# Performance work log

Measured on AMD Instinct MI355X. Metric: run time of the kernel, lower is better.

## Reference

```python
import jax, jax.numpy as jnp
import numpy as np

B, T, C_IN = 2, 4096, 1024
INTER, OUT = 1024, 1024
ROPE_DIM = 64
GAMMA = 0.99609375  # 1 - 2**-8
GROUPS = 32
EPS = 1e-6


def setup_inputs() -> dict:
    key = jax.random.key(0)
    k = jax.random.split(key, 4)
    return {
        "X_Q": jax.random.normal(k[0], (B, T, C_IN), dtype=jnp.float32),
        "W_Q": jax.random.normal(k[1], (C_IN, INTER), dtype=jnp.float32) / C_IN,
        "W_K": jax.random.normal(k[2], (C_IN, INTER), dtype=jnp.float32) / C_IN,
        "W_V": jax.random.normal(k[3], (C_IN, OUT), dtype=jnp.float32) / C_IN,
        "gn_weight": jnp.ones((OUT,), dtype=jnp.float32),
        "gn_bias": jnp.zeros((OUT,), dtype=jnp.float32),
    }


def _rope(x):
    # lucidrains RotaryEmbedding: rotate first ROPE_DIM features, pairwise-adjacent
    t = x.shape[-2]
    inv_freq = 1.0 / (10000.0 ** (jnp.arange(0, ROPE_DIM, 2, dtype=jnp.float32) / ROPE_DIM))
    freqs = jnp.arange(t, dtype=jnp.float32)[:, None] * inv_freq[None, :]  # [T, ROPE_DIM/2]
    freqs = jnp.repeat(freqs, 2, axis=-1)                                   # [T, ROPE_DIM]
    cos, sin = jnp.cos(freqs), jnp.sin(freqs)
    xr, xp = x[..., :ROPE_DIM], x[..., ROPE_DIM:]
    x1, x2 = xr[..., 0::2], xr[..., 1::2]
    rot = jnp.stack([-x2, x1], axis=-1).reshape(xr.shape)  # rotate_half (adjacent pairs)
    return jnp.concatenate([xr * cos + rot * sin, xp], axis=-1)


def _group_norm(x, w, b):
    # torch GroupNorm applied on x.reshape(-1, C)
    sh = x.shape
    c = sh[-1]
    xr = x.reshape(-1, GROUPS, c // GROUPS)
    mu = xr.mean(-1, keepdims=True)
    var = xr.var(-1, keepdims=True)
    xn = ((xr - mu) * jax.lax.rsqrt(var + EPS)).reshape(-1, c)
    return (xn * w + b).reshape(sh)


def reference(X_Q, W_Q, W_K, W_V, gn_weight, gn_bias):
    Q = jax.nn.silu(_rope(X_Q @ W_Q))  # [B,T,INTER]
    K = jax.nn.silu(_rope(X_Q @ W_K))
    V = jax.nn.silu(X_Q @ W_V)         # [B,T,OUT]
    A = jnp.einsum('btd,bsd->bts', Q, K)  # [B,T,T]
    # decay mask: original multiplies by _get_D(gamma,T).T -> gamma^(m-n) for m>=n
    n = jnp.arange(T)[:, None]
    m = jnp.arange(T)[None, :]
    upper = m >= n
    Dt = jnp.where(upper, GAMMA ** jnp.where(upper, m - n, 0).astype(jnp.float32), 0.0)
    A = A * Dt
    out = jnp.einsum('bts,bsd->btd', A, V)  # [B,T,OUT]
    # dropout p=0 (eval) -> identity
    return _group_norm(out, gn_weight, gn_bias)
```

## Files before the change

kernel.cpp:

```cpp
#include <hip/hip_runtime.h>


typedef __attribute__((ext_vector_type(8))) short bf16x8;
typedef __attribute__((ext_vector_type(4))) short bf16x4;
typedef __attribute__((ext_vector_type(4))) float f32x4;

#define MFMA16(a, b, c) __builtin_amdgcn_mfma_f32_16x16x32_bf16(a, b, c, 0, 0, 0)

static __device__ __forceinline__ short f2bf(float f) {
  unsigned u = __builtin_bit_cast(unsigned, f);
  u = (u + 0x7fffu + ((u >> 16) & 1u)) >> 16;
  return (short)u;
}

static __device__ __forceinline__ float fast_silu(float v) {
  return v * __builtin_amdgcn_rcpf(1.f + __expf(-v));
}

static __device__ __forceinline__ void gl_lds16(const void* g, void* l) {
  __builtin_amdgcn_global_load_lds(
      (const __attribute__((address_space(1))) void*)g,
      (__attribute__((address_space(3))) void*)l, 16, 0, 0);
}

static __device__ __forceinline__ int swzc(int col, int row) {
  return (((col >> 3) ^ (row & 7)) << 3) | (col & 7);
}

#define T_LEN 4096
#define CIN 1024

#define LOG2G (-0.0056465633f)
#define L2IF (0.41524101f)

__global__ __launch_bounds__(256)
void prep_kernel(const float* __restrict__ X, short* __restrict__ Xb,
                 const float* __restrict__ Wq, const float* __restrict__ Wk,
                 const float* __restrict__ Wv, short* __restrict__ WT) {
  __shared__ short tile[64][72];
  const int bx = blockIdx.x;
  const int tid = threadIdx.x;
  if (bx < 4096) {
    const int gid = bx * 256 + tid;
    const int row = gid >> 7;
    const int c = gid & 127;
    const float* s = &X[(size_t)gid * 8];
    float4 f0 = *(const float4*)s;
    float4 f1 = *(const float4*)(s + 4);
    bf16x8 v = {f2bf(f0.x), f2bf(f0.y), f2bf(f0.z), f2bf(f0.w),
                f2bf(f1.x), f2bf(f1.y), f2bf(f1.z), f2bf(f1.w)};
    const int pc = (c & 0x78) | ((c ^ row) & 7);
    *(bf16x8*)&Xb[(size_t)row * 1024 + pc * 8] = v;
    return;
  }
  const int bx2 = bx - 4096;
  const int k0 = (bx2 & 15) * 64, n0 = ((bx2 >> 4) & 15) * 64, mat = bx2 >> 8;
  const float* __restrict__ W = (mat == 0) ? Wq : (mat == 1) ? Wk : Wv;
  const int r = tid >> 4, c = tid & 15;
#pragma unroll
  for (int i = 0; i < 4; ++i) {
    int row = r + 16 * i;
    float4 f = *(const float4*)&W[(size_t)(k0 + row) * CIN + n0 + c * 4];
    tile[c * 4 + 0][row] = f2bf(f.x);
    tile[c * 4 + 1][row] = f2bf(f.y);
    tile[c * 4 + 2][row] = f2bf(f.z);
    tile[c * 4 + 3][row] = f2bf(f.w);
  }
  __syncthreads();
  const int n = tid >> 2, seg = tid & 3;
  bf16x8 lo = *(const bf16x8*)&tile[n][seg * 16];
  bf16x8 hi = *(const bf16x8*)&tile[n][seg * 16 + 8];
  const int R = mat * 1024 + n0 + n;
  const int a0 = (k0 >> 3) + seg * 2;
  short* base = &WT[(size_t)R * CIN];
  *(bf16x8*)&base[(a0 ^ (n & 7)) * 8] = lo;
  *(bf16x8*)&base[((a0 + 1) ^ (n & 7)) * 8] = hi;
}

#define GEMM_DECLS()                                   \
  const int tid = threadIdx.x;                         \
  const int lane = tid & 63, wave = tid >> 6;          \
  const int wm = wave >> 1, wn = wave & 1;             \
  const int l15 = lane & 15, quad = lane >> 4;         \
  const int srow = tid >> 3;                           \
  const int scol = (tid & 7) * 8;                      \
  const int asw = (l15 & 7);

#define ACC_INIT4(acc)                                 \
  _Pragma("unroll") for (int i = 0; i < 4; ++i)        \
  _Pragma("unroll") for (int j = 0; j < 4; ++j) {      \
    f32x4 z = {0.f, 0.f, 0.f, 0.f};                    \
    acc[i][j] = z;                                     \
  }

#define STAGE_TILE(dst, src, ld, r0, k0, nrows)        \
  _Pragma("unroll") for (int i = 0; i < (nrows) / 32; ++i) \
    gl_lds16(&src[(size_t)((r0) + i * 32 + srow) * (ld) + (k0) + scol], \
             &dst[i * 32 + srow][scol]);

#define FRAG_MFMA44(As, Bs, acc)                                            \
  {                                                                         \
    bf16x8 af[4][2], bfr[4][2];                                             \
    _Pragma("unroll") for (int im = 0; im < 4; ++im)                        \
    _Pragma("unroll") for (int ks = 0; ks < 2; ++ks)                        \
      af[im][ks] = *(const bf16x8*)&As[wm * 64 + im * 16 + l15]             \
                       [((ks * 4 + quad) ^ asw) * 8];                       \
    _Pragma("unroll") for (int in = 0; in < 4; ++in)                        \
    _Pragma("unroll") for (int ks = 0; ks < 2; ++ks)                        \
      bfr[in][ks] = *(const bf16x8*)&Bs[wn * 64 + in * 16 + l15]            \
                        [((ks * 4 + quad) ^ asw) * 8];                      \
    _Pragma("unroll") for (int ks = 0; ks < 2; ++ks)                        \
    _Pragma("unroll") for (int im = 0; im < 4; ++im)                        \
    _Pragma("unroll") for (int in = 0; in < 4; ++in)                        \
      acc[im][in] = MFMA16(af[im][ks], bfr[in][ks], acc[im][in]);           \
  }

__global__ __launch_bounds__(256, 2)
void qkv_gemm(const short* __restrict__ Xb, const short* __restrict__ WT,
              short* __restrict__ Qb, short* __restrict__ Kb,
              short* __restrict__ Vt) {
  __shared__ __align__(16) short As[128][64];
  __shared__ __align__(16) short Bs[128][64];
  GEMM_DECLS();
  const int m0 = blockIdx.x * 128;
  const int c0 = blockIdx.y * 128;

  f32x4 acc[4][4];
  ACC_INIT4(acc);

  for (int k0 = 0; k0 < CIN; k0 += 64) {
    __syncthreads();
    STAGE_TILE(As, Xb, CIN, m0, k0, 128);
    STAGE_TILE(Bs, WT, CIN, c0, k0, 128);
    __syncthreads();
    FRAG_MFMA44(As, Bs, acc);
  }

  const int mat = (c0 >> 10);
  const bool ropeBlk = (mat < 2) && ((c0 & 1023) == 0);
#pragma unroll
  for (int im = 0; im < 4; ++im) {
#pragma unroll
    for (int in = 0; in < 4; ++in) {
      const int c = c0 + wn * 64 + in * 16 + l15;
      const int colm = c & 1023;
      const int mbase = m0 + wm * 64 + im * 16 + quad * 4;
      short vv[4];
      if (ropeBlk && colm < 64) {
        const float invf = exp2f(-L2IF * (float)(colm >> 1));
#pragma unroll
        for (int r = 0; r < 4; ++r) {
          float v = acc[im][in][r];
          int t = (mbase + r) & (T_LEN - 1);
          float partner = __shfl_xor(v, 1, 64);
          float ang = (float)t * invf;
          float s_ = __sinf(ang), c_ = __cosf(ang);
          v = (colm & 1) ? (v * c_ + partner * s_) : (v * c_ - partner * s_);
          vv[r] = f2bf(fast_silu(v));
        }
      } else {
#pragma unroll
        for (int r = 0; r < 4; ++r) vv[r] = f2bf(fast_silu(acc[im][in][r]));
      }
      if (mat == 0) {
#pragma unroll
        for (int r = 0; r < 4; ++r)
          Qb[(size_t)(mbase + r) * 1024 + swzc(colm, mbase + r)] = vv[r];
      } else if (mat == 1) {
#pragma unroll
        for (int r = 0; r < 4; ++r)
          Kb[(size_t)(mbase + r) * 1024 + swzc(colm, mbase + r)] = vv[r];
      } else {
        bf16x4 v4 = {vv[0], vv[1], vv[2], vv[3]};
        *(bf16x4*)&Vt[(size_t)colm * 8192 +
                      (((mbase >> 3) ^ (colm & 7)) << 3) + (mbase & 7)] = v4;
      }
    }
  }
}

__global__ __launch_bounds__(256, 2)
void score_kernel(const short* __restrict__ Qb, const short* __restrict__ Kb,
                  short* __restrict__ Ab) {
  int idx = blockIdx.x;
  int ti = 0;
  while (idx >= 32 - ti) { idx -= 32 - ti; ++ti; }
  const int si = ti + idx;
  const int b = blockIdx.y;
  const int s0 = si * 128, t0 = ti * 128;

  __shared__ __align__(16) short Qs[128][64];
  __shared__ __align__(16) short Ks[128][64];
  GEMM_DECLS();

  f32x4 acc[4][4];
  ACC_INIT4(acc);

  for (int k0 = 0; k0 < 1024; k0 += 64) {
    __syncthreads();
    STAGE_TILE(Qs, Qb, 1024, b * T_LEN + t0, k0, 128);
    STAGE_TILE(Ks, Kb, 1024, b * T_LEN + s0, k0, 128);
    __syncthreads();
    FRAG_MFMA44(Qs, Ks, acc);
  }

#pragma unroll
  for (int im = 0; im < 4; ++im) {
#pragma unroll
    for (int in = 0; in < 4; ++in) {
      int s = s0 + wn * 64 + in * 16 + l15;
#pragma unroll
      for (int r = 0; r < 4; ++r) {
        int t = t0 + wm * 64 + im * 16 + quad * 4 + r;
        int d = s - t;
        float v = acc[im][in][r];
        v = (d < 0) ? 0.f : v * exp2f((float)d * LOG2G);
        Ab[((size_t)(b * T_LEN + t)) * T_LEN + swzc(s, t)] = f2bf(v);
      }
    }
  }
}

__global__ __launch_bounds__(512, 2)
void av_kernel(const short* __restrict__ Ab, const short* __restrict__ Vt,
               const float* __restrict__ gw, const float* __restrict__ gb,
               float* __restrict__ Out) {
  const int p = blockIdx.x, b = blockIdx.y, di = blockIdx.z;
  const int n0 = di * 128;

  __shared__ __align__(16) short As2[128][64];
  __shared__ __align__(16) short Vs[128][64];

  const int tid = threadIdx.x;
  const int lane = tid & 63, wave = tid >> 6;
  const int wm = wave >> 2, wn = wave & 3;
  const int l15 = lane & 15, quad = lane >> 4;
  const int srow = tid >> 3;
  const int scol = (tid & 7) * 8;
  const int asw = l15 & 7;

  float w2[2], b2[2];
#pragma unroll
  for (int in = 0; in < 2; ++in) {
    int n = n0 + wn * 32 + in * 16 + l15;
    w2[in] = gw[n];
    b2[in] = gb[n];
  }

#pragma unroll 1
  for (int half = 0; half < 2; ++half) {
    const int ti2 = half ? (31 - p) : p;
    const int t0 = ti2 * 128;
    const int nIt = (T_LEN - t0) >> 6;

    f32x4 acc[4][2];
#pragma unroll
    for (int i = 0; i < 4; ++i)
#pragma unroll
      for (int j = 0; j < 2; ++j) {
        f32x4 z = {0.f, 0.f, 0.f, 0.f};
        acc[i][j] = z;
      }

#pragma unroll 1
    for (int it = 0; it < nIt; ++it) {
      const int s = t0 + (it << 6);
      __syncthreads();
      gl_lds16(&Ab[(size_t)(b * T_LEN + t0 + srow) * T_LEN + s + scol],
               &As2[srow][scol]);
      gl_lds16(&Ab[(size_t)(b * T_LEN + t0 + 64 + srow) * T_LEN + s + scol],
               &As2[64 + srow][scol]);
      gl_lds16(&Vt[(size_t)(n0 + srow) * 8192 + b * T_LEN + s + scol],
               &Vs[srow][scol]);
      gl_lds16(&Vt[(size_t)(n0 + 64 + srow) * 8192 + b * T_LEN + s + scol],
               &Vs[64 + srow][scol]);
      __syncthreads();

      bf16x8 af[4][2], bfr[2][2];
#pragma unroll
      for (int im = 0; im < 4; ++im)
#pragma unroll
        for (int ks = 0; ks < 2; ++ks)
          af[im][ks] = *(const bf16x8*)&As2[wm * 64 + im * 16 + l15]
                           [((ks * 4 + quad) ^ asw) * 8];
#pragma unroll
      for (int in = 0; in < 2; ++in)
#pragma unroll
        for (int ks = 0; ks < 2; ++ks)
          bfr[in][ks] = *(const bf16x8*)&Vs[wn * 32 + in * 16 + l15]
                            [((ks * 4 + quad) ^ asw) * 8];
#pragma unroll
      for (int ks = 0; ks < 2; ++ks)
#pragma unroll
        for (int im = 0; im < 4; ++im)
#pragma unroll
          for (int in = 0; in < 2; ++in)
            acc[im][in] = MFMA16(af[im][ks], bfr[in][ks], acc[im][in]);
    }

#pragma unroll
    for (int im = 0; im < 4; ++im) {
#pragma unroll
      for (int r = 0; r < 4; ++r) {
        int t = t0 + wm * 64 + im * 16 + quad * 4 + r;
        float* orow = &Out[((size_t)(b * T_LEN + t)) * 1024];
        float a0 = acc[im][0][r], a1 = acc[im][1][r];
        float s = a0 + a1;
        float q = a0 * a0 + a1 * a1;
        s += __shfl_xor(s, 1, 64);
        q += __shfl_xor(q, 1, 64);
        s += __shfl_xor(s, 2, 64);
        q += __shfl_xor(q, 2, 64);
        s += __shfl_xor(s, 4, 64);
        q += __shfl_xor(q, 4, 64);
        s += __shfl_xor(s, 8, 64);
        q += __shfl_xor(q, 8, 64);
        float mean = s * (1.f / 32.f);
        float var = q * (1.f / 32.f) - mean * mean;
        float rstd = rsqrtf(var + 1e-6f);
        int n = n0 + wn * 32 + l15;
        orow[n] = (a0 - mean) * rstd * w2[0] + b2[0];
        orow[n + 16] = (a1 - mean) * rstd * w2[1] + b2[1];
      }
    }
  }
}

extern "C" void kernel_launch(void* const* d_in, const int* in_sizes, int n_in,
                              void* d_out, int out_size, void* d_ws,
                              size_t ws_size, hipStream_t stream) {
  const float* X = (const float*)d_in[0];
  const float* Wq = (const float*)d_in[1];
  const float* Wk = (const float*)d_in[2];
  const float* Wv = (const float*)d_in[3];
  const float* gw = (const float*)d_in[4];
  const float* gb = (const float*)d_in[5];
  float* Out = (float*)d_out;

  short* Qb = (short*)d_ws;
  short* Kb = Qb + (size_t)8192 * 1024;
  short* Vt = Kb + (size_t)8192 * 1024;
  short* Ab = Vt + (size_t)8192 * 1024;
  short* Xb = Ab;
  short* WT = Xb + (size_t)8192 * 1024;

  prep_kernel<<<4864, 256, 0, stream>>>(X, Xb, Wq, Wk, Wv, WT);
  qkv_gemm<<<dim3(64, 24), 256, 0, stream>>>(Xb, WT, Qb, Kb, Vt);
  score_kernel<<<dim3(528, 2), 256, 0, stream>>>(Qb, Kb, Ab);
  av_kernel<<<dim3(16, 2, 8), 512, 0, stream>>>(Ab, Vt, gw, gb, Out);
}
```

Before: 281.4 us.

## Triple-buffer AV kernel loads and widen score kernel K-tile to 128

The AV kernel now keeps a three-stage LDS ring for the A and V tiles. Loads for iteration it+2 are issued asynchronously via global_load_lds, and partial vmcnt waits let global latency overlap with the MFMA work. This triples shared memory per block, so launch bounds drop to one block per SIMD slot, which lowers occupancy. The score kernel stages 128-wide K slices with direct global-to-LDS loads in place of the old macro, halving the number of barrier round-trips at the cost of more LDS.

```diff
diff --git a/kernel.cpp b/kernel.cpp
--- a/kernel.cpp
+++ b/kernel.cpp
@@ -189,19 +189,48 @@
   const int b = blockIdx.y;
   const int s0 = si * 128, t0 = ti * 128;
 
-  __shared__ __align__(16) short Qs[128][64];
-  __shared__ __align__(16) short Ks[128][64];
-  GEMM_DECLS();
+  __shared__ __align__(16) short Qs[128][128];
+  __shared__ __align__(16) short Ks[128][128];
+
+  const int tid = threadIdx.x;
+  const int lane = tid & 63, wave = tid >> 6;
+  const int wm = wave >> 1, wn = wave & 1;
+  const int l15 = lane & 15, quad = lane >> 4;
+  const int srow2 = tid >> 4;
+  const int scol2 = (tid & 15) * 8;
+  const int asw = l15 & 7;
 
   f32x4 acc[4][4];
   ACC_INIT4(acc);
 
-  for (int k0 = 0; k0 < 1024; k0 += 64) {
+#pragma unroll 1
+  for (int k0 = 0; k0 < 1024; k0 += 128) {
     __syncthreads();
-    STAGE_TILE(Qs, Qb, 1024, b * T_LEN + t0, k0, 128);
-    STAGE_TILE(Ks, Kb, 1024, b * T_LEN + s0, k0, 128);
+#pragma unroll
+    for (int i = 0; i < 8; ++i) {
+      gl_lds16(&Qb[(size_t)(b * T_LEN + t0 + i * 16 + srow2) * 1024 + k0 + scol2],
+               &Qs[i * 16 + srow2][scol2]);
+      gl_lds16(&Kb[(size_t)(b * T_LEN + s0 + i * 16 + srow2) * 1024 + k0 + scol2],
+               &Ks[i * 16 + srow2][scol2]);
+    }
     __syncthreads();
-    FRAG_MFMA44(Qs, Ks, acc);
+#pragma unroll
+    for (int ks = 0; ks < 4; ++ks) {
+      bf16x8 af[4], bfr[4];
+#pragma unroll
+      for (int im = 0; im < 4; ++im)
+        af[im] = *(const bf16x8*)&Qs[wm * 64 + im * 16 + l15]
+                     [((ks * 4 + quad) ^ asw) * 8];
+#pragma unroll
+      for (int in = 0; in < 4; ++in)
+        bfr[in] = *(const bf16x8*)&Ks[wn * 64 + in * 16 + l15]
+                      [((ks * 4 + quad) ^ asw) * 8];
+#pragma unroll
+      for (int im = 0; im < 4; ++im)
+#pragma unroll
+        for (int in = 0; in < 4; ++in)
+          acc[im][in] = MFMA16(af[im], bfr[in], acc[im][in]);
+    }
   }
 
 #pragma unroll
@@ -221,15 +250,15 @@
   }
 }
 
-__global__ __launch_bounds__(512, 2)
+__global__ __launch_bounds__(512, 1)
 void av_kernel(const short* __restrict__ Ab, const short* __restrict__ Vt,
                const float* __restrict__ gw, const float* __restrict__ gb,
                float* __restrict__ Out) {
   const int p = blockIdx.x, b = blockIdx.y, di = blockIdx.z;
   const int n0 = di * 128;
 
-  __shared__ __align__(16) short As2[128][64];
-  __shared__ __align__(16) short Vs[128][64];
+  __shared__ __align__(16) short As2[3][128][64];
+  __shared__ __align__(16) short Vs[3][128][64];
 
   const int tid = threadIdx.x;
   const int lane = tid & 63, wave = tid >> 6;
@@ -247,6 +276,18 @@
     b2[in] = gb[n];
   }
 
+#define AV_STAGE(buf, s)                                                      \
+  {                                                                           \
+    gl_lds16(&Ab[(size_t)(b * T_LEN + t0 + srow) * T_LEN + (s) + scol],       \
+             &As2[buf][srow][scol]);                                          \
+    gl_lds16(&Ab[(size_t)(b * T_LEN + t0 + 64 + srow) * T_LEN + (s) + scol],  \
+             &As2[buf][64 + srow][scol]);                                     \
+    gl_lds16(&Vt[(size_t)(n0 + srow) * 8192 + b * T_LEN + (s) + scol],        \
+             &Vs[buf][srow][scol]);                                           \
+    gl_lds16(&Vt[(size_t)(n0 + 64 + srow) * 8192 + b * T_LEN + (s) + scol],   \
+             &Vs[buf][64 + srow][scol]);                                      \
+  }
+
 #pragma unroll 1
   for (int half = 0; half < 2; ++half) {
     const int ti2 = half ? (31 - p) : p;
@@ -262,32 +303,38 @@
         acc[i][j] = z;
       }
 
+    __syncthreads();
+    AV_STAGE(0, t0);
+    AV_STAGE(1, t0 + 64);
+
+    int cur = 0;
 #pragma unroll 1
     for (int it = 0; it < nIt; ++it) {
-      const int s = t0 + (it << 6);
-      __syncthreads();
-      gl_lds16(&Ab[(size_t)(b * T_LEN + t0 + srow) * T_LEN + s + scol],
-               &As2[srow][scol]);
-      gl_lds16(&Ab[(size_t)(b * T_LEN + t0 + 64 + srow) * T_LEN + s + scol],
-               &As2[64 + srow][scol]);
-      gl_lds16(&Vt[(size_t)(n0 + srow) * 8192 + b * T_LEN + s + scol],
-               &Vs[srow][scol]);
-      gl_lds16(&Vt[(size_t)(n0 + 64 + srow) * 8192 + b * T_LEN + s + scol],
-               &Vs[64 + srow][scol]);
-      __syncthreads();
+      __builtin_amdgcn_s_barrier();
+      const int nx2 = (cur >= 1) ? cur - 1 : 2;
+      if (it + 2 < nIt) {
+        const int s = t0 + ((it + 2) << 6);
+        AV_STAGE(nx2, s);
+        asm volatile("s_waitcnt vmcnt(8)" ::: "memory");
+      } else if (it + 1 < nIt) {
+        asm volatile("s_waitcnt vmcnt(4)" ::: "memory");
+      } else {
+        asm volatile("s_waitcnt vmcnt(0)" ::: "memory");
+      }
+      __builtin_amdgcn_s_barrier();
 
       bf16x8 af[4][2], bfr[2][2];
 #pragma unroll
       for (int im = 0; im < 4; ++im)
 #pragma unroll
         for (int ks = 0; ks < 2; ++ks)
-          af[im][ks] = *(const bf16x8*)&As2[wm * 64 + im * 16 + l15]
+          af[im][ks] = *(const bf16x8*)&As2[cur][wm * 64 + im * 16 + l15]
                            [((ks * 4 + quad) ^ asw) * 8];
 #pragma unroll
       for (int in = 0; in < 2; ++in)
 #pragma unroll
         for (int ks = 0; ks < 2; ++ks)
-          bfr[in][ks] = *(const bf16x8*)&Vs[wn * 32 + in * 16 + l15]
+          bfr[in][ks] = *(const bf16x8*)&Vs[cur][wn * 32 + in * 16 + l15]
                             [((ks * 4 + quad) ^ asw) * 8];
 #pragma unroll
       for (int ks = 0; ks < 2; ++ks)
@@ -296,6 +343,8 @@
 #pragma unroll
           for (int in = 0; in < 2; ++in)
             acc[im][in] = MFMA16(af[im][ks], bfr[in][ks], acc[im][in]);
+
+      cur = (cur == 2) ? 0 : cur + 1;
     }
 
 #pragma unroll
@@ -324,6 +373,7 @@
       }
     }
   }
+#undef AV_STAGE
 }
 
 extern "C" void kernel_launch(void* const* d_in, const int* in_sizes, int n_in,
```

After: 283.3 us. No clear change (+0.7%).
